# Optimization experiments

Hardware: AMD Instinct MI355X
Metric: run time of the kernel (lower is better)

The kernel has to match this reference:

```python
import jax, jax.numpy as jnp
import numpy as np

N, F_IN, H = 8192, 128, 256
AVG_DEG_P = 16.0 / N  # ~16 neighbors per node, BA-graph-like sparsity


def setup_inputs() -> dict:
    key = jax.random.key(0)
    ks = jax.random.split(key, 16)
    # symmetric 0/1 adjacency, no self-loops
    B = jax.random.bernoulli(ks[0], AVG_DEG_P, (N, N)).astype(jnp.float32)
    A = jnp.maximum(B, B.T)
    A = A * (1.0 - jnp.eye(N, dtype=jnp.float32))
    features = jax.random.normal(ks[1], (N, F_IN), dtype=jnp.float32)
    treatments = jax.random.bernoulli(ks[2], 0.1, (N, 1)).astype(jnp.float32)
    def glorot(k, shape):
        lim = float(np.sqrt(6.0 / (shape[0] + shape[1])))
        return jax.random.uniform(k, shape, jnp.float32, -lim, lim)
    return {
        "A": A,
        "features": features,
        "treatments": treatments,
        "W1": glorot(ks[3], (F_IN, H)),   # GCNConv layer 1 weight
        "b1": jnp.zeros((H,), jnp.float32),
        "W2": glorot(ks[4], (H, H)),      # GCNConv layer 2 weight
        "b2": jnp.zeros((H,), jnp.float32),
        "W_emb": glorot(ks[5], (H + 1, H)),
        "b_emb": jnp.zeros((H,), jnp.float32),
        "W_t0": glorot(ks[6], (H, 1)),
        "b_t0": jnp.zeros((1,), jnp.float32),
        "W_t1": glorot(ks[7], (H, 1)),
        "b_t1": jnp.zeros((1,), jnp.float32),
    }


def _gcn_norm(A):
    # PyG GCNConv default: D^-1/2 (A + I) D^-1/2
    A_hat = A + jnp.eye(A.shape[0], dtype=A.dtype)
    d = jnp.sum(A_hat, axis=1)
    dinv = jnp.where(d > 0, 1.0 / jnp.sqrt(d), 0.0)
    return A_hat * dinv[:, None] * dinv[None, :]


def reference(A, features, treatments, W1, b1, W2, b2, W_emb, b_emb, W_t0, b_t0, W_t1, b_t1):
    nA = _gcn_norm(A)                                  # [N, N]
    h = jax.nn.relu(nA @ (features @ W1) + b1)         # GCNConv 1, [N, H]
    h = jax.nn.relu(nA @ (h @ W2) + b2)                # GCNConv 2, [N, H]
    deg = jnp.sum(A, axis=1) + 1e-8                    # [N]
    # faithful to torch: (A * treatments).sum(dim=1) broadcasts treatments[N,1] over columns
    exposure = (jnp.sum(A * treatments, axis=1) / deg)[:, None]  # [N, 1]
    rep = jnp.concatenate([h, exposure], axis=1)       # [N, H+1]
    emb = jax.nn.relu(rep @ W_emb + b_emb)             # [N, H]
    y0_pred = (emb @ W_t0 + b_t0).reshape(-1)          # [N]
    y1_pred = (emb @ W_t1 + b_t1).reshape(-1)          # [N]
    return (y0_pred, y1_pred, emb)
```

## Files before the change

kernel.cpp:

```cpp
#include <hip/hip_runtime.h>

#define NN   8192
#define FIN  128
#define HH   256
#define CAP  128

__global__ __launch_bounds__(256) void k_build(
    const float* __restrict__ A, const float* __restrict__ treat,
    int* __restrict__ cols, int* __restrict__ cnt,
    float* __restrict__ dinv, float* __restrict__ expo)
{
  const int row = blockIdx.x;
  const float4* Ar = reinterpret_cast<const float4*>(A + (size_t)row * NN);
  __shared__ int s_cnt;
  __shared__ float s_rs[4];
  if (threadIdx.x == 0) s_cnt = 0;
  __syncthreads();

  float rs = 0.f;
  int* myCols = cols + (size_t)row * CAP;
  #pragma unroll
  for (int it = 0; it < NN / 4 / 256; ++it) {
    const int idx = it * 256 + threadIdx.x;
    const float4 a = Ar[idx];
    const int base = idx * 4;
    const float av[4] = {a.x, a.y, a.z, a.w};
    #pragma unroll
    for (int u = 0; u < 4; ++u) {
      if (av[u] != 0.0f) {
        rs += av[u];
        int p = atomicAdd(&s_cnt, 1);
        if (p < CAP) myCols[p] = base + u;
      }
    }
  }
  #pragma unroll
  for (int off = 32; off > 0; off >>= 1) rs += __shfl_down(rs, off);
  const int wid = threadIdx.x >> 6;
  if ((threadIdx.x & 63) == 0) s_rs[wid] = rs;
  __syncthreads();
  if (threadIdx.x == 0) {
    const float R = s_rs[0] + s_rs[1] + s_rs[2] + s_rs[3];
    int n = s_cnt; if (n > CAP) n = CAP;
    cnt[row]  = n;
    dinv[row] = rsqrtf(R + 1.0f);
    expo[row] = treat[row] * R / (R + 1e-8f);
  }
}

template<int K, bool EXPO>
__global__ __launch_bounds__(256) void k_gemm(
    const float* __restrict__ M, const float* __restrict__ W,
    const float* __restrict__ bias, const float* __restrict__ expo,
    float* __restrict__ out)
{
  constexpr int BM = 128, BN = 64, KT = 16;
  __shared__ float As[KT][BM];
  __shared__ float Bs[KT][BN];
  const int tid = threadIdx.x;
  const int tx = tid & 15;
  const int ty = tid >> 4;
  const int r0 = blockIdx.x * BM;
  const int c0 = blockIdx.y * BN;

  float acc[8][4];
  #pragma unroll
  for (int i = 0; i < 8; ++i)
    #pragma unroll
    for (int j = 0; j < 4; ++j) acc[i][j] = 0.f;

  const int lr = tid >> 1;
  const int lk = (tid & 1) * 8;
  const int bk = tid >> 4;
  const int bc = (tid & 15) * 4;

  for (int k0 = 0; k0 < K; k0 += KT) {
    const float4 a0 = *reinterpret_cast<const float4*>(&M[(size_t)(r0 + lr) * K + k0 + lk]);
    const float4 a1 = *reinterpret_cast<const float4*>(&M[(size_t)(r0 + lr) * K + k0 + lk + 4]);
    const float4 b0 = *reinterpret_cast<const float4*>(&W[(size_t)(k0 + bk) * HH + c0 + bc]);
    __syncthreads();
    As[lk + 0][lr] = a0.x; As[lk + 1][lr] = a0.y; As[lk + 2][lr] = a0.z; As[lk + 3][lr] = a0.w;
    As[lk + 4][lr] = a1.x; As[lk + 5][lr] = a1.y; As[lk + 6][lr] = a1.z; As[lk + 7][lr] = a1.w;
    *reinterpret_cast<float4*>(&Bs[bk][bc]) = b0;
    __syncthreads();
    #pragma unroll
    for (int kk = 0; kk < KT; ++kk) {
      const float4 av0 = *reinterpret_cast<const float4*>(&As[kk][ty * 8]);
      const float4 av1 = *reinterpret_cast<const float4*>(&As[kk][ty * 8 + 4]);
      const float4 bv  = *reinterpret_cast<const float4*>(&Bs[kk][tx * 4]);
      const float ar[8] = {av0.x, av0.y, av0.z, av0.w, av1.x, av1.y, av1.z, av1.w};
      const float br[4] = {bv.x, bv.y, bv.z, bv.w};
      #pragma unroll
      for (int i = 0; i < 8; ++i)
        #pragma unroll
        for (int j = 0; j < 4; ++j)
          acc[i][j] += ar[i] * br[j];
    }
  }

  float eb[4] = {0, 0, 0, 0}, bs[4] = {0, 0, 0, 0};
  if constexpr (EXPO) {
    const float4 we = *reinterpret_cast<const float4*>(&W[(size_t)K * HH + c0 + tx * 4]);
    eb[0] = we.x; eb[1] = we.y; eb[2] = we.z; eb[3] = we.w;
    const float4 bv = *reinterpret_cast<const float4*>(&bias[c0 + tx * 4]);
    bs[0] = bv.x; bs[1] = bv.y; bs[2] = bv.z; bs[3] = bv.w;
  }
  #pragma unroll
  for (int i = 0; i < 8; ++i) {
    const int r = r0 + ty * 8 + i;
    float4 o;
    float ov[4];
    if constexpr (EXPO) {
      const float e = expo[r];
      #pragma unroll
      for (int j = 0; j < 4; ++j) ov[j] = fmaxf(acc[i][j] + e * eb[j] + bs[j], 0.f);
    } else {
      #pragma unroll
      for (int j = 0; j < 4; ++j) ov[j] = acc[i][j];
    }
    o.x = ov[0]; o.y = ov[1]; o.z = ov[2]; o.w = ov[3];
    *reinterpret_cast<float4*>(&out[(size_t)r * HH + c0 + tx * 4]) = o;
  }
}

__global__ __launch_bounds__(256) void k_agg(
    const float* __restrict__ M,
    const int* __restrict__ cols, const int* __restrict__ cnt,
    const float* __restrict__ dinv, const float* __restrict__ bias,
    float* __restrict__ out)
{
  const int i = blockIdx.x;
  const int c = threadIdx.x;
  __shared__ int   s_cols[CAP];
  __shared__ float s_w[CAP];
  const int n = cnt[i];
  for (int t = threadIdx.x; t < n; t += 256) {
    const int j = cols[(size_t)i * CAP + t];
    s_cols[t] = j;
    s_w[t] = dinv[j];
  }
  __syncthreads();
  const float di = dinv[i];
  float acc = di * M[(size_t)i * HH + c];
  #pragma unroll 4
  for (int t = 0; t < n; ++t)
    acc += s_w[t] * M[(size_t)s_cols[t] * HH + c];
  const float v = di * acc + bias[c];
  out[(size_t)i * HH + c] = fmaxf(v, 0.f);
}

__global__ __launch_bounds__(64) void k_heads(
    const float* __restrict__ emb,
    const float* __restrict__ Wt0, const float* __restrict__ bt0,
    const float* __restrict__ Wt1, const float* __restrict__ bt1,
    float* __restrict__ y0, float* __restrict__ y1)
{
  const int i = blockIdx.x;
  const int l = threadIdx.x;
  float s0 = 0.f, s1 = 0.f;
  #pragma unroll
  for (int c = l; c < HH; c += 64) {
    const float e = emb[(size_t)i * HH + c];
    s0 += e * Wt0[c];
    s1 += e * Wt1[c];
  }
  #pragma unroll
  for (int off = 32; off > 0; off >>= 1) {
    s0 += __shfl_down(s0, off);
    s1 += __shfl_down(s1, off);
  }
  if (l == 0) {
    y0[i] = s0 + bt0[0];
    y1[i] = s1 + bt1[0];
  }
}

extern "C" void kernel_launch(void* const* d_in, const int* in_sizes, int n_in,
                              void* d_out, int out_size, void* d_ws, size_t ws_size,
                              hipStream_t stream)
{
  const float* A      = (const float*)d_in[0];
  const float* feats  = (const float*)d_in[1];
  const float* treat  = (const float*)d_in[2];
  const float* W1     = (const float*)d_in[3];
  const float* b1     = (const float*)d_in[4];
  const float* W2     = (const float*)d_in[5];
  const float* b2     = (const float*)d_in[6];
  const float* W_emb  = (const float*)d_in[7];
  const float* b_emb  = (const float*)d_in[8];
  const float* W_t0   = (const float*)d_in[9];
  const float* b_t0   = (const float*)d_in[10];
  const float* W_t1   = (const float*)d_in[11];
  const float* b_t1   = (const float*)d_in[12];
  float* dout = (float*)d_out;

  int*   cols = (int*)d_ws;
  int*   cnt  = cols + (size_t)NN * CAP;
  float* dinv = (float*)(cnt + NN);
  float* expo = dinv + NN;
  float* bufA = expo + NN;
  float* bufB = bufA + (size_t)NN * HH;

  float* y0  = dout;
  float* y1  = dout + NN;
  float* emb = dout + 2 * NN;

  const dim3 gemmGrid(NN / 128, HH / 64);

  k_build<<<NN, 256, 0, stream>>>(A, treat, cols, cnt, dinv, expo);
  k_gemm<FIN, false><<<gemmGrid, 256, 0, stream>>>(feats, W1, nullptr, nullptr, bufA);
  k_agg<<<NN, 256, 0, stream>>>(bufA, cols, cnt, dinv, b1, bufB);
  k_gemm<HH, false><<<gemmGrid, 256, 0, stream>>>(bufB, W2, nullptr, nullptr, bufA);
  k_agg<<<NN, 256, 0, stream>>>(bufA, cols, cnt, dinv, b2, bufB);
  k_gemm<HH, true><<<gemmGrid, 256, 0, stream>>>(bufB, W_emb, b_emb, expo, emb);
  k_heads<<<NN, 64, 0, stream>>>(emb, W_t0, b_t0, W_t1, b_t1, y0, y1);
}
```

Baseline: 519.0 us.

## Fuse build with first GEMM, fuse heads into final GEMM, widen aggregation

```diff
diff --git a/kernel.cpp b/kernel.cpp
--- a/kernel.cpp
+++ b/kernel.cpp
@@ -5,16 +5,19 @@
 #define HH   256
 #define CAP  128
 
-__global__ __launch_bounds__(256) void k_build(
-    const float* __restrict__ A, const float* __restrict__ treat,
+typedef float f32x4 __attribute__((ext_vector_type(4)));
+
+__device__ __forceinline__ const f32x4* c4(const float* p) { return (const f32x4*)p; }
+__device__ __forceinline__       f32x4* p4(float* p)       { return (f32x4*)p; }
+
+__device__ __forceinline__ void build_body(
+    int row, const float* __restrict__ A, const float* __restrict__ treat,
     int* __restrict__ cols, int* __restrict__ cnt,
-    float* __restrict__ dinv, float* __restrict__ expo)
-{
-  const int row = blockIdx.x;
-  const float4* Ar = reinterpret_cast<const float4*>(A + (size_t)row * NN);
-  __shared__ int s_cnt;
-  __shared__ float s_rs[4];
-  if (threadIdx.x == 0) s_cnt = 0;
+    float* __restrict__ dinv, float* __restrict__ expo,
+    int* s_cnt, float* s_rs)
+{
+  const f32x4* Ar = c4(A + (size_t)row * NN);
+  if (threadIdx.x == 0) *s_cnt = 0;
   __syncthreads();
 
   float rs = 0.f;
@@ -22,14 +25,13 @@
   #pragma unroll
   for (int it = 0; it < NN / 4 / 256; ++it) {
     const int idx = it * 256 + threadIdx.x;
-    const float4 a = Ar[idx];
+    const f32x4 a = __builtin_nontemporal_load(Ar + idx);
     const int base = idx * 4;
-    const float av[4] = {a.x, a.y, a.z, a.w};
     #pragma unroll
     for (int u = 0; u < 4; ++u) {
-      if (av[u] != 0.0f) {
-        rs += av[u];
-        int p = atomicAdd(&s_cnt, 1);
+      if (a[u] != 0.0f) {
+        rs += a[u];
+        int p = atomicAdd(s_cnt, 1);
         if (p < CAP) myCols[p] = base + u;
       }
     }
@@ -41,138 +43,181 @@
   __syncthreads();
   if (threadIdx.x == 0) {
     const float R = s_rs[0] + s_rs[1] + s_rs[2] + s_rs[3];
-    int n = s_cnt; if (n > CAP) n = CAP;
+    int n = *s_cnt; if (n > CAP) n = CAP;
     cnt[row]  = n;
     dinv[row] = rsqrtf(R + 1.0f);
     expo[row] = treat[row] * R / (R + 1e-8f);
   }
 }
 
-template<int K, bool EXPO>
+template<int K, bool EXPO, bool HEADS>
+__device__ __forceinline__ void gemm_body(
+    int bidx,
+    const float* __restrict__ M, const float* __restrict__ W,
+    const float* __restrict__ bias, const float* __restrict__ expo,
+    const float* __restrict__ Wt0, const float* __restrict__ Wt1,
+    float* __restrict__ out, float* __restrict__ y0, float* __restrict__ y1,
+    float (*As)[64], float (*Bs)[64])
+{
+  const int tid = threadIdx.x;
+  const int tx = tid & 15, ty = tid >> 4;
+  const int bx = bidx & 127, by = bidx >> 7;
+  const int r0 = bx * 64, c0 = by * 64;
+  const int la_r = tid & 63;
+  const int la_k = (tid >> 6) << 2;
+  const int lb_k = tid >> 4;
+  const int lb_c = (tid & 15) << 2;
+
+  const float* Abase = M + (size_t)(r0 + la_r) * K + la_k;
+  const float* Bbase = W + (size_t)lb_k * HH + c0 + lb_c;
+
+  f32x4 aR = *c4(Abase);
+  f32x4 bR = *c4(Bbase);
+  float acc[4][4] = {};
+
+  #pragma unroll 1
+  for (int k0 = 0; k0 < K; k0 += 16) {
+    As[la_k + 0][la_r] = aR[0];
+    As[la_k + 1][la_r] = aR[1];
+    As[la_k + 2][la_r] = aR[2];
+    As[la_k + 3][la_r] = aR[3];
+    *p4(&Bs[lb_k][lb_c]) = bR;
+    __syncthreads();
+    if (k0 + 16 < K) {
+      aR = *c4(Abase + k0 + 16);
+      bR = *c4(Bbase + (size_t)(k0 + 16) * HH);
+    }
+    #pragma unroll
+    for (int kk = 0; kk < 16; ++kk) {
+      const f32x4 av = *c4(&As[kk][ty * 4]);
+      const f32x4 bv = *c4(&Bs[kk][tx * 4]);
+      #pragma unroll
+      for (int i = 0; i < 4; ++i)
+        #pragma unroll
+        for (int j = 0; j < 4; ++j)
+          acc[i][j] += av[i] * bv[j];
+    }
+    __syncthreads();
+  }
+
+  f32x4 eb = {0.f, 0.f, 0.f, 0.f}, bs = {0.f, 0.f, 0.f, 0.f};
+  if constexpr (EXPO) {
+    eb = *c4(&W[(size_t)K * HH + c0 + tx * 4]);
+    bs = *c4(&bias[c0 + tx * 4]);
+  }
+  f32x4 wt0 = {0.f, 0.f, 0.f, 0.f}, wt1 = {0.f, 0.f, 0.f, 0.f};
+  if constexpr (HEADS) {
+    wt0 = *c4(&Wt0[c0 + tx * 4]);
+    wt1 = *c4(&Wt1[c0 + tx * 4]);
+  }
+  #pragma unroll
+  for (int i = 0; i < 4; ++i) {
+    const int r = r0 + ty * 4 + i;
+    f32x4 o;
+    if constexpr (EXPO) {
+      const float e = expo[r];
+      #pragma unroll
+      for (int j = 0; j < 4; ++j) o[j] = fmaxf(acc[i][j] + e * eb[j] + bs[j], 0.f);
+    } else {
+      #pragma unroll
+      for (int j = 0; j < 4; ++j) o[j] = acc[i][j];
+    }
+    *p4(&out[(size_t)r * HH + c0 + tx * 4]) = o;
+    if constexpr (HEADS) {
+      float s0 = o[0] * wt0[0] + o[1] * wt0[1] + o[2] * wt0[2] + o[3] * wt0[3];
+      float s1 = o[0] * wt1[0] + o[1] * wt1[1] + o[2] * wt1[2] + o[3] * wt1[3];
+      #pragma unroll
+      for (int off = 8; off > 0; off >>= 1) {
+        s0 += __shfl_down(s0, off);
+        s1 += __shfl_down(s1, off);
+      }
+      if ((tid & 15) == 0) {
+        atomicAdd(&y0[r], s0);
+        atomicAdd(&y1[r], s1);
+      }
+    }
+  }
+}
+
+__global__ __launch_bounds__(256) void k_build_gemm1(
+    const float* __restrict__ A, const float* __restrict__ treat,
+    const float* __restrict__ feats, const float* __restrict__ W1,
+    int* __restrict__ cols, int* __restrict__ cnt,
+    float* __restrict__ dinv, float* __restrict__ expo,
+    float* __restrict__ bufA)
+{
+  __shared__ float As[16][64];
+  __shared__ float Bs[16][64];
+  __shared__ int   s_cnt;
+  __shared__ float s_rs[4];
+  const int b = blockIdx.x;
+  if (b < 512) {
+    gemm_body<FIN, false, false>(b, feats, W1, nullptr, nullptr, nullptr, nullptr,
+                                 bufA, nullptr, nullptr, As, Bs);
+  } else {
+    build_body(b - 512, A, treat, cols, cnt, dinv, expo, &s_cnt, s_rs);
+  }
+}
+
+template<int K, bool EXPO, bool HEADS>
 __global__ __launch_bounds__(256) void k_gemm(
     const float* __restrict__ M, const float* __restrict__ W,
     const float* __restrict__ bias, const float* __restrict__ expo,
-    float* __restrict__ out)
-{
-  constexpr int BM = 128, BN = 64, KT = 16;
-  __shared__ float As[KT][BM];
-  __shared__ float Bs[KT][BN];
-  const int tid = threadIdx.x;
-  const int tx = tid & 15;
-  const int ty = tid >> 4;
-  const int r0 = blockIdx.x * BM;
-  const int c0 = blockIdx.y * BN;
-
-  float acc[8][4];
-  #pragma unroll
-  for (int i = 0; i < 8; ++i)
-    #pragma unroll
-    for (int j = 0; j < 4; ++j) acc[i][j] = 0.f;
-
-  const int lr = tid >> 1;
-  const int lk = (tid & 1) * 8;
-  const int bk = tid >> 4;
-  const int bc = (tid & 15) * 4;
-
-  for (int k0 = 0; k0 < K; k0 += KT) {
-    const float4 a0 = *reinterpret_cast<const float4*>(&M[(size_t)(r0 + lr) * K + k0 + lk]);
-    const float4 a1 = *reinterpret_cast<const float4*>(&M[(size_t)(r0 + lr) * K + k0 + lk + 4]);
-    const float4 b0 = *reinterpret_cast<const float4*>(&W[(size_t)(k0 + bk) * HH + c0 + bc]);
-    __syncthreads();
-    As[lk + 0][lr] = a0.x; As[lk + 1][lr] = a0.y; As[lk + 2][lr] = a0.z; As[lk + 3][lr] = a0.w;
-    As[lk + 4][lr] = a1.x; As[lk + 5][lr] = a1.y; As[lk + 6][lr] = a1.z; As[lk + 7][lr] = a1.w;
-    *reinterpret_cast<float4*>(&Bs[bk][bc]) = b0;
-    __syncthreads();
-    #pragma unroll
-    for (int kk = 0; kk < KT; ++kk) {
-      const float4 av0 = *reinterpret_cast<const float4*>(&As[kk][ty * 8]);
-      const float4 av1 = *reinterpret_cast<const float4*>(&As[kk][ty * 8 + 4]);
-      const float4 bv  = *reinterpret_cast<const float4*>(&Bs[kk][tx * 4]);
-      const float ar[8] = {av0.x, av0.y, av0.z, av0.w, av1.x, av1.y, av1.z, av1.w};
-      const float br[4] = {bv.x, bv.y, bv.z, bv.w};
-      #pragma unroll
-      for (int i = 0; i < 8; ++i)
-        #pragma unroll
-        for (int j = 0; j < 4; ++j)
-          acc[i][j] += ar[i] * br[j];
-    }
-  }
-
-  float eb[4] = {0, 0, 0, 0}, bs[4] = {0, 0, 0, 0};
-  if constexpr (EXPO) {
-    const float4 we = *reinterpret_cast<const float4*>(&W[(size_t)K * HH + c0 + tx * 4]);
-    eb[0] = we.x; eb[1] = we.y; eb[2] = we.z; eb[3] = we.w;
-    const float4 bv = *reinterpret_cast<const float4*>(&bias[c0 + tx * 4]);
-    bs[0] = bv.x; bs[1] = bv.y; bs[2] = bv.z; bs[3] = bv.w;
-  }
-  #pragma unroll
-  for (int i = 0; i < 8; ++i) {
-    const int r = r0 + ty * 8 + i;
-    float4 o;
-    float ov[4];
-    if constexpr (EXPO) {
-      const float e = expo[r];
-      #pragma unroll
-      for (int j = 0; j < 4; ++j) ov[j] = fmaxf(acc[i][j] + e * eb[j] + bs[j], 0.f);
-    } else {
-      #pragma unroll
-      for (int j = 0; j < 4; ++j) ov[j] = acc[i][j];
-    }
-    o.x = ov[0]; o.y = ov[1]; o.z = ov[2]; o.w = ov[3];
-    *reinterpret_cast<float4*>(&out[(size_t)r * HH + c0 + tx * 4]) = o;
-  }
-}
-
+    const float* __restrict__ Wt0, const float* __restrict__ Wt1,
+    float* __restrict__ out, float* __restrict__ y0, float* __restrict__ y1)
+{
+  __shared__ float As[16][64];
+  __shared__ float Bs[16][64];
+  gemm_body<K, EXPO, HEADS>(blockIdx.x, M, W, bias, expo, Wt0, Wt1, out, y0, y1, As, Bs);
+}
+
+template<bool INIT>
 __global__ __launch_bounds__(256) void k_agg(
     const float* __restrict__ M,
     const int* __restrict__ cols, const int* __restrict__ cnt,
     const float* __restrict__ dinv, const float* __restrict__ bias,
-    float* __restrict__ out)
-{
-  const int i = blockIdx.x;
-  const int c = threadIdx.x;
-  __shared__ int   s_cols[CAP];
-  __shared__ float s_w[CAP];
+    float* __restrict__ out,
+    float* __restrict__ dout, const float* __restrict__ bt0, const float* __restrict__ bt1)
+{
+  const int wid  = threadIdx.x >> 6;
+  const int lane = threadIdx.x & 63;
+  const int i    = blockIdx.x * 4 + wid;
+  __shared__ int   s_cols[4][CAP];
+  __shared__ float s_w[4][CAP];
+
+  if constexpr (INIT) {
+    if (blockIdx.x < 64) {
+      const int idx = blockIdx.x * 256 + threadIdx.x;
+      dout[idx] = (idx < NN) ? bt0[0] : bt1[0];
+    }
+  }
+
   const int n = cnt[i];
-  for (int t = threadIdx.x; t < n; t += 256) {
-    const int j = cols[(size_t)i * CAP + t];
-    s_cols[t] = j;
-    s_w[t] = dinv[j];
+  if (lane < n) {
+    const int j = cols[(size_t)i * CAP + lane];
+    s_cols[wid][lane] = j;  s_w[wid][lane] = dinv[j];
+  }
+  if (lane + 64 < n) {
+    const int j = cols[(size_t)i * CAP + lane + 64];
+    s_cols[wid][lane + 64] = j;  s_w[wid][lane + 64] = dinv[j];
   }
   __syncthreads();
+
   const float di = dinv[i];
-  float acc = di * M[(size_t)i * HH + c];
+  const f32x4 bias4 = *c4(&bias[lane * 4]);
+  f32x4 acc = *c4(&M[(size_t)i * HH + lane * 4]);
+  acc *= di;
   #pragma unroll 4
-  for (int t = 0; t < n; ++t)
-    acc += s_w[t] * M[(size_t)s_cols[t] * HH + c];
-  const float v = di * acc + bias[c];
-  out[(size_t)i * HH + c] = fmaxf(v, 0.f);
-}
-
-__global__ __launch_bounds__(64) void k_heads(
-    const float* __restrict__ emb,
-    const float* __restrict__ Wt0, const float* __restrict__ bt0,
-    const float* __restrict__ Wt1, const float* __restrict__ bt1,
-    float* __restrict__ y0, float* __restrict__ y1)
-{
-  const int i = blockIdx.x;
-  const int l = threadIdx.x;
-  float s0 = 0.f, s1 = 0.f;
-  #pragma unroll
-  for (int c = l; c < HH; c += 64) {
-    const float e = emb[(size_t)i * HH + c];
-    s0 += e * Wt0[c];
-    s1 += e * Wt1[c];
-  }
-  #pragma unroll
-  for (int off = 32; off > 0; off >>= 1) {
-    s0 += __shfl_down(s0, off);
-    s1 += __shfl_down(s1, off);
-  }
-  if (l == 0) {
-    y0[i] = s0 + bt0[0];
-    y1[i] = s1 + bt1[0];
-  }
+  for (int t = 0; t < n; ++t) {
+    const int   j = s_cols[wid][t];
+    const float w = s_w[wid][t];
+    const f32x4 v = *c4(&M[(size_t)j * HH + lane * 4]);
+    acc += w * v;
+  }
+  f32x4 o = di * acc + bias4;
+  #pragma unroll
+  for (int q = 0; q < 4; ++q) o[q] = fmaxf(o[q], 0.f);
+  *p4(&out[(size_t)i * HH + lane * 4]) = o;
 }
 
 extern "C" void kernel_launch(void* const* d_in, const int* in_sizes, int n_in,
@@ -205,13 +250,13 @@
   float* y1  = dout + NN;
   float* emb = dout + 2 * NN;
 
-  const dim3 gemmGrid(NN / 128, HH / 64);
-
-  k_build<<<NN, 256, 0, stream>>>(A, treat, cols, cnt, dinv, expo);
-  k_gemm<FIN, false><<<gemmGrid, 256, 0, stream>>>(feats, W1, nullptr, nullptr, bufA);
-  k_agg<<<NN, 256, 0, stream>>>(bufA, cols, cnt, dinv, b1, bufB);
-  k_gemm<HH, false><<<gemmGrid, 256, 0, stream>>>(bufB, W2, nullptr, nullptr, bufA);
-  k_agg<<<NN, 256, 0, stream>>>(bufA, cols, cnt, dinv, b2, bufB);
-  k_gemm<HH, true><<<gemmGrid, 256, 0, stream>>>(bufB, W_emb, b_emb, expo, emb);
-  k_heads<<<NN, 64, 0, stream>>>(emb, W_t0, b_t0, W_t1, b_t1, y0, y1);
-}
+  k_build_gemm1<<<8704, 256, 0, stream>>>(A, treat, feats, W1, cols, cnt, dinv, expo, bufA);
+  k_agg<false><<<NN / 4, 256, 0, stream>>>(bufA, cols, cnt, dinv, b1, bufB,
+                                           nullptr, nullptr, nullptr);
+  k_gemm<HH, false, false><<<512, 256, 0, stream>>>(bufB, W2, nullptr, nullptr,
+                                                    nullptr, nullptr, bufA, nullptr, nullptr);
+  k_agg<true><<<NN / 4, 256, 0, stream>>>(bufA, cols, cnt, dinv, b2, bufB,
+                                          dout, b_t0, b_t1);
+  k_gemm<HH, true, true><<<512, 256, 0, stream>>>(bufB, W_emb, b_emb, expo,
+                                                  W_t0, W_t1, emb, y0, y1);
+}
```

Result: faster. 458.4 us (-11.7%).
